# Kernel optimization log

Measured on AMD Instinct MI355X. Metric: run time of the kernel, lower is better.

## Reference

```python
import jax, jax.numpy as jnp
import numpy as np

N_NODES = 100000
N_EDGES = 1600000
D_NODE = 32
D_EDGE = 16
D_HID = 64
D_OUT = 32


def setup_inputs() -> dict:
    key = jax.random.key(0)
    ks = jax.random.split(key, 7)
    x = jax.random.normal(ks[0], (N_NODES, D_NODE), dtype=jnp.float32)
    edge_index = jax.random.randint(ks[1], (2, N_EDGES), 0, N_NODES, dtype=jnp.int64)
    edge_attr = jax.random.normal(ks[2], (N_EDGES, D_EDGE), dtype=jnp.float32)
    # 2-layer MLP params (Linear -> ReLU -> Linear), He-ish scaling
    W1 = jax.random.normal(ks[3], (D_NODE + D_EDGE, D_HID), dtype=jnp.float32) * (2.0 / (D_NODE + D_EDGE)) ** 0.5
    b1 = jnp.zeros((D_HID,), dtype=jnp.float32)
    W2 = jax.random.normal(ks[4], (D_HID, D_OUT), dtype=jnp.float32) * (2.0 / D_HID) ** 0.5
    b2 = jnp.zeros((D_OUT,), dtype=jnp.float32)
    return {"x": x, "edge_index": edge_index, "edge_attr": edge_attr,
            "W1": W1, "b1": b1, "W2": W2, "b2": b2}


def reference(x, edge_index, edge_attr, W1, b1, W2, b2):
    row, col = edge_index[0], edge_index[1]
    # gather source-node feats and concat with edge feats: [E, d_node + d_edge]
    inp = jnp.concatenate([x[col], edge_attr], axis=1)
    # 2-layer MLP over edges
    h = jax.nn.relu(inp @ W1 + b1)
    messages = h @ W2 + b2  # [E, d_out]
    # scatter-sum aggregate by destination node
    message = jax.ops.segment_sum(messages, row, num_segments=x.shape[0])
    return message
```

## Files before the change

kernel.cpp:

```cpp
#include <hip/hip_runtime.h>
#include <hip/hip_bf16.h>
#include <stdint.h>

#define N_NODES 100000
#define N_EDGES 1600000
#define D_NODE  32
#define D_EDGE  16
#define D_IN    48
#define D_HID   64
#define D_OUT   32

#define NBKT 98
#define BCAP 18432
#define SLICES (BCAP / 256)
#define S1_EDGES 1024
#define S1_NB 1563
#define SCAN_NB 391

#define CHUNKS_PER_BLOCK 4
#define BPB (SLICES / CHUNKS_PER_BLOCK)
#define MAXB_PER_XCD 13
#define AGG_GRID (8 * MAXB_PER_XCD * BPB)

#define NFLAGS_OFF  ((size_t)0)
#define NB1_OFF     ((size_t)64)
#define NB2_OFF     ((size_t)320)
#define W1BF_OFF    ((size_t)1024)
#define W2BF_OFF    ((size_t)9216)
#define GCUR_OFF    ((size_t)16384)
#define XBF_OFF     ((size_t)65536)
#define TMPH_OFF    ((size_t)8388608)
#define TMPE_OFF    ((size_t)16777216)
#define REC_OFF     ((size_t)75497472)
#define ACCUM_OFF   ((size_t)90177536)

typedef __attribute__((ext_vector_type(8))) short bf16x8;
typedef __attribute__((ext_vector_type(4))) float f32x4;

__device__ inline float bf2f(unsigned int u16) {
    return __uint_as_float(u16 << 16);
}
__device__ inline unsigned short f2bf_rne(float f) {
    unsigned int x = __float_as_uint(f);
    unsigned int r = (x + 0x7FFFu + ((x >> 16) & 1u)) >> 16;
    return (unsigned short)r;
}
__device__ inline unsigned int pk_bf2(float a, float b) {
    float2 f; f.x = a; f.y = b;
    __hip_bfloat162 h = __float22bfloat162_rn(f);
    return *reinterpret_cast<unsigned int*>(&h);
}
__device__ inline float ld_f(const void* p, int i, int isbf) {
    if (isbf) return bf2f(((const unsigned short*)p)[i]);
    return ((const float*)p)[i];
}

__global__ __launch_bounds__(256) void prep_kernel(
        const void* __restrict__ xq, const void* __restrict__ idxq,
        const void* __restrict__ W1q, const void* __restrict__ b1q,
        const void* __restrict__ W2q, const void* __restrict__ b2q,
        char* __restrict__ ws) {
    const int t = threadIdx.x;
    const int i0 = blockIdx.x * 256 + t;

    __shared__ int s_isbf;
    if (t < 64) {
        unsigned short u = ((const unsigned short*)xq)[t];
        unsigned long long mb = __ballot(((u >> 7) & 0xFF) >= 140);
        if (t == 0) s_isbf = (mb == 0ULL);
    }

    float4* acc4 = (float4*)(ws + ACCUM_OFF);
    float4 z; z.x = z.y = z.z = z.w = 0.0f;
    for (int i = i0; i < (N_NODES + 1) * 32 / 4; i += SCAN_NB * 256) acc4[i] = z;

    __syncthreads();
    const int isbf = s_isbf;

    unsigned short* xbf = (unsigned short*)(ws + XBF_OFF);
    for (int i = i0; i < N_NODES * 32 / 8; i += SCAN_NB * 256) {
        uint4 o;
        if (isbf) {
            o = ((const uint4*)xq)[i];
        } else {
            const float4* xp = (const float4*)xq + i * 2;
            float4 a = xp[0], b = xp[1];
            o.x = pk_bf2(a.x, a.y); o.y = pk_bf2(a.z, a.w);
            o.z = pk_bf2(b.x, b.y); o.w = pk_bf2(b.z, b.w);
        }
        ((uint4*)xbf)[i] = o;
    }

    if (blockIdx.x != 0) return;

    if (t < NBKT) ((int*)(ws + GCUR_OFF))[t] = t * BCAP;
    if (t < 64) {
        int wodd = ((const int*)idxq)[2 * t + 1];
        unsigned long long mi = __ballot(wodd != 0);
        if (t == 0) {
            int* flags = (int*)(ws + NFLAGS_OFF);
            flags[0] = isbf;
            flags[1] = (mi == 0ULL);
        }
    }

    float* b1 = (float*)(ws + NB1_OFF);
    float* b2 = (float*)(ws + NB2_OFF);
    unsigned short* w1b = (unsigned short*)(ws + W1BF_OFF);
    unsigned short* w2b = (unsigned short*)(ws + W2BF_OFF);

    if (t < D_HID) b1[t] = ld_f(b1q, t, isbf);
    if (t < D_OUT) b2[t] = ld_f(b2q, t, isbf);

    for (int i = t; i < D_HID * 64; i += 256) {
        int n = i >> 6, k = i & 63;
        float v = (k < D_IN) ? ld_f(W1q, k * D_HID + n, isbf) : 0.0f;
        w1b[i] = f2bf_rne(v);
    }
    for (int i = t; i < D_OUT * 64; i += 256) {
        int n = i >> 6, k = i & 63;
        w2b[i] = f2bf_rne(ld_f(W2q, k * D_OUT + n, isbf));
    }
}

#define PIDX(s) ((s) + ((s) >> 3))
__global__ __launch_bounds__(512) void partition_kernel(
        const void* __restrict__ idxq, const void* __restrict__ eaq,
        char* __restrict__ ws) {
    const int is64 = ((const int*)(ws + NFLAGS_OFF))[1];
    const int isbf = ((const int*)(ws + NFLAGS_OFF))[0];
    __shared__ int hist[128];
    __shared__ int sc[128];
    __shared__ int lofs[128];
    __shared__ int base[128];
    __shared__ int lcur[128];
    __shared__ unsigned int hdr[S1_EDGES];
    __shared__ unsigned char bkt[S1_EDGES];
    __shared__ __align__(16) uint4 pay[2][S1_EDGES + (S1_EDGES >> 3)];

    const int t = threadIdx.x;
    if (t < 128) hist[t] = 0;
    __syncthreads();

    const int e0 = blockIdx.x * S1_EDGES;
    const int total = min(N_EDGES - e0, S1_EDGES);

    int dstv[2];
#pragma unroll
    for (int i = 0; i < 2; ++i) {
        const int e = e0 + i * 512 + t;
        int dst = -1;
        if (e < N_EDGES) {
            if (is64) dst = (int)((const long long*)idxq)[e];
            else      dst = ((const int*)idxq)[e];
            atomicAdd(&hist[dst >> 10], 1);
        }
        dstv[i] = dst;
    }
    __syncthreads();

    if (t < 128) sc[t] = hist[t];
    __syncthreads();
    for (int d = 1; d < 128; d <<= 1) {
        int a = 0;
        if (t < 128 && t >= d) a = sc[t - d];
        __syncthreads();
        if (t < 128) sc[t] += a;
        __syncthreads();
    }
    if (t < 128) {
        lofs[t] = sc[t] - hist[t];
        lcur[t] = 0;
        if (t < NBKT) base[t] = atomicAdd((int*)(ws + GCUR_OFF) + t, hist[t]);
    }
    __syncthreads();

#pragma unroll
    for (int i = 0; i < 2; ++i) {
        const int e = e0 + i * 512 + t;
        if (e >= N_EDGES) continue;
        const int dst = dstv[i];
        int src;
        if (is64) src = (int)((const long long*)idxq)[N_EDGES + e];
        else      src = ((const int*)idxq)[N_EDGES + e];
        const int b = dst >> 10;
        const int r = atomicAdd(&lcur[b], 1);
        const int s = lofs[b] + r;
        hdr[s] = (unsigned)src | ((unsigned)(dst & 1023) << 17);
        bkt[s] = (unsigned char)b;

        uint4 u0, u1;
        if (isbf) {
            const uint4* p = (const uint4*)((const unsigned short*)eaq + (size_t)e * 16);
            u0 = p[0]; u1 = p[1];
        } else {
            const float4* p = (const float4*)((const float*)eaq + (size_t)e * 16);
            float4 a = p[0], b4 = p[1], c = p[2], d = p[3];
            u0.x = pk_bf2(a.x, a.y);  u0.y = pk_bf2(a.z, a.w);
            u0.z = pk_bf2(b4.x, b4.y); u0.w = pk_bf2(b4.z, b4.w);
            u1.x = pk_bf2(c.x, c.y);  u1.y = pk_bf2(c.z, c.w);
            u1.z = pk_bf2(d.x, d.y);  u1.w = pk_bf2(d.z, d.w);
        }
        pay[0][PIDX(s)] = u0;
        pay[1][PIDX(s)] = u1;
    }
    __syncthreads();

    unsigned int* tmph = (unsigned int*)(ws + TMPH_OFF);
    uint4*        tmp4 = (uint4*)(ws + TMPE_OFF);
    for (int s = t; s < total; s += 512) {
        const int b = bkt[s];
        const size_t g = (size_t)base[b] + (s - lofs[b]);
        tmph[g] = hdr[s];
        tmp4[g * 2]     = pay[0][PIDX(s)];
        tmp4[g * 2 + 1] = pay[1][PIDX(s)];
    }
}

__global__ __launch_bounds__(1024) void sort_kernel(char* __restrict__ ws) {
    __shared__ int hist[1024];
    __shared__ int cur[1024];
    const int b = blockIdx.x;
    const int t = threadIdx.x;
    hist[t] = 0;
    __syncthreads();

    const int cnt = ((const int*)(ws + GCUR_OFF))[b] - b * BCAP;
    const unsigned int* tmph = (const unsigned int*)(ws + TMPH_OFF) + (size_t)b * BCAP;
    unsigned long long* rec = (unsigned long long*)(ws + REC_OFF) + (size_t)b * BCAP;

    for (int i = t; i < cnt; i += 1024)
        atomicAdd(&hist[(tmph[i] >> 17) & 1023], 1);
    __syncthreads();

    int v = hist[t];
    for (int d = 1; d < 1024; d <<= 1) {
        int a = (t >= d) ? hist[t - d] : 0;
        __syncthreads();
        hist[t] += a;
        __syncthreads();
    }
    cur[t] = hist[t] - v;
    __syncthreads();

    for (int i = t; i < cnt; i += 1024) {
        unsigned int h = tmph[i];
        const int rd = (h >> 17) & 1023;
        const int rk = atomicAdd(&cur[rd], 1);
        unsigned long long out = ((unsigned long long)rd << 32)
                               | ((unsigned long long)(unsigned)i << 17)
                               | (h & 0x1FFFFu);
        rec[rk] = out;
    }
}

__global__ __launch_bounds__(256) void edge_mlp_agg_kernel(
        const char* __restrict__ wsro,
        float* __restrict__ accum) {
    const int xcd = blockIdx.x & 7;
    const int j   = blockIdx.x >> 3;
    const int m   = j / BPB;
    const int nb  = 12 + (xcd < 2);
    if (m >= nb) return;
    const int b      = xcd + (m << 3);
    const int slice0 = (j % BPB) * CHUNKS_PER_BLOCK;

    const int cnt = ((const int*)(wsro + GCUR_OFF))[b] - b * BCAP;
    if (slice0 * 256 >= cnt) return;

    __shared__ __align__(16) unsigned short hbuf[4][2][16][72];

    const int w   = threadIdx.x >> 6;
    const int l   = threadIdx.x & 63;
    const int m16 = l & 15;
    const int q   = l >> 4;

    const unsigned short* w1b = (const unsigned short*)(wsro + W1BF_OFF);
    const unsigned short* w2b = (const unsigned short*)(wsro + W2BF_OFF);
    const float* b1 = (const float*)(wsro + NB1_OFF);
    const float* b2 = (const float*)(wsro + NB2_OFF);
    const unsigned short* xbf  = (const unsigned short*)(wsro + XBF_OFF);
    const unsigned short* tmpe = (const unsigned short*)(wsro + TMPE_OFF) + (size_t)b * BCAP * 16;
    const unsigned long long* rec = (const unsigned long long*)(wsro + REC_OFF) + (size_t)b * BCAP;

    bf16x8 w1f[4][2], w2f[2][2];
#pragma unroll
    for (int t = 0; t < 4; ++t)
#pragma unroll
        for (int c = 0; c < 2; ++c)
            w1f[t][c] = *(const bf16x8*)(w1b + ((t * 16 + m16) * 64 + c * 32 + q * 8));
#pragma unroll
    for (int t = 0; t < 2; ++t)
#pragma unroll
        for (int c = 0; c < 2; ++c)
            w2f[t][c] = *(const bf16x8*)(w2b + ((t * 16 + m16) * 64 + c * 32 + q * 8));

    const float b1v[4] = { b1[m16], b1[16 + m16], b1[32 + m16], b1[48 + m16] };
    const float b2v[2] = { b2[m16], b2[16 + m16] };
    const int n0 = b << 10;

    for (int cc = 0; cc < CHUNKS_PER_BLOCK; ++cc) {
        const int kb = (slice0 + cc) * 256 + w * 64;
        if ((slice0 + cc) * 256 >= cnt) break;

        int srcv[4], tixv[4], dstv[4];
#pragma unroll
        for (int g = 0; g < 4; ++g) {
            const int p = kb + g * 16 + m16;
            unsigned long long r = rec[p];
            if (p < cnt) {
                unsigned int lo = (unsigned int)r;
                srcv[g] = (int)(lo & 0x1FFFFu);
                tixv[g] = (int)(lo >> 17);
                dstv[g] = n0 + (int)(r >> 32);
            } else {
                srcv[g] = 0;
                tixv[g] = 0;
                dstv[g] = N_NODES;
            }
        }

        bf16x8 A0[4], A1[4];
#pragma unroll
        for (int g = 0; g < 4; ++g) {
            A0[g] = *(const bf16x8*)(xbf  + (size_t)srcv[g] * D_NODE + q * 8);
            A1[g] = *(const bf16x8*)(tmpe + (size_t)tixv[g] * 16 + (q & 1) * 8);
        }

        auto L1 = [&](int g, int bb) {
#pragma unroll
            for (int t = 0; t < 4; ++t) {
                f32x4 c;
                c[0] = c[1] = c[2] = c[3] = b1v[t];
                c = __builtin_amdgcn_mfma_f32_16x16x32_bf16(A0[g], w1f[t][0], c, 0, 0, 0);
                c = __builtin_amdgcn_mfma_f32_16x16x32_bf16(A1[g], w1f[t][1], c, 0, 0, 0);
                unsigned int u0 = pk_bf2(fmaxf(c[0], 0.0f), fmaxf(c[1], 0.0f));
                unsigned int u1 = pk_bf2(fmaxf(c[2], 0.0f), fmaxf(c[3], 0.0f));
                hbuf[w][bb][q * 4 + 0][t * 16 + m16] = (unsigned short)u0;
                hbuf[w][bb][q * 4 + 1][t * 16 + m16] = (unsigned short)(u0 >> 16);
                hbuf[w][bb][q * 4 + 2][t * 16 + m16] = (unsigned short)u1;
                hbuf[w][bb][q * 4 + 3][t * 16 + m16] = (unsigned short)(u1 >> 16);
            }
        };

        auto L2R = [&](int g, int bb) {
            bf16x8 a20 = *(const bf16x8*)(&hbuf[w][bb][m16][q * 8]);
            bf16x8 a21 = *(const bf16x8*)(&hbuf[w][bb][m16][32 + q * 8]);
            f32x4 c0, c1;
            c0[0] = c0[1] = c0[2] = c0[3] = b2v[0];
            c1[0] = c1[1] = c1[2] = c1[3] = b2v[1];
            c0 = __builtin_amdgcn_mfma_f32_16x16x32_bf16(a20, w2f[0][0], c0, 0, 0, 0);
            c0 = __builtin_amdgcn_mfma_f32_16x16x32_bf16(a21, w2f[0][1], c0, 0, 0, 0);
            c1 = __builtin_amdgcn_mfma_f32_16x16x32_bf16(a20, w2f[1][0], c1, 0, 0, 0);
            c1 = __builtin_amdgcn_mfma_f32_16x16x32_bf16(a21, w2f[1][1], c1, 0, 0, 0);

            const int dstw = dstv[g];
            int dprev = __shfl(dstw, (m16 + 15) & 15, 16);
            bool isStart = (m16 == 0) || (dprev != dstw);
            unsigned long long bal = __ballot(isStart);
            unsigned mask16 = (unsigned)(bal >> (l & 48)) & 0xFFFFu;
            int start = 0;
            while (start < 16) {
                unsigned rest = mask16 >> 1 >> start;
                int next = rest ? (start + 1 + (int)__builtin_ctz(rest)) : 16;
                int d = __shfl(dstw, start, 16);
                float s0 = 0.0f, s1 = 0.0f;
#pragma unroll
                for (int r = 0; r < 4; ++r) {
                    int mm = q * 4 + r;
                    bool in = (mm >= start) && (mm < next);
                    s0 += in ? c0[r] : 0.0f;
                    s1 += in ? c1[r] : 0.0f;
                }
                s0 += __shfl_xor(s0, 16); s0 += __shfl_xor(s0, 32);
                s1 += __shfl_xor(s1, 16); s1 += __shfl_xor(s1, 32);
                if (q == 0) {
                    unsafeAtomicAdd(accum + (size_t)d * 32 + m16,      s0);
                    unsafeAtomicAdd(accum + (size_t)d * 32 + 16 + m16, s1);
                }
                start = next;
            }
        };

        L1(0, 0);
        L1(1, 1);
        L2R(0, 0);
        L1(2, 0);
        L2R(1, 1);
        L1(3, 1);
        L2R(2, 0);
        L2R(3, 1);
    }
}

__global__ __launch_bounds__(256) void convert_kernel(
        const char* __restrict__ wsro, const float* __restrict__ accum,
        void* __restrict__ out) {
    const int isbf = ((const int*)(wsro + NFLAGS_OFF))[0];
    const int i = blockIdx.x * 256 + threadIdx.x;
    float4 v = ((const float4*)accum)[i];
    if (isbf) {
        uint2 u;
        u.x = pk_bf2(v.x, v.y);
        u.y = pk_bf2(v.z, v.w);
        ((uint2*)out)[i] = u;
    } else {
        ((float4*)out)[i] = v;
    }
}

extern "C" void kernel_launch(void* const* d_in, const int* in_sizes, int n_in,
                              void* d_out, int out_size, void* d_ws, size_t ws_size,
                              hipStream_t stream) {
    const void* x   = d_in[0];
    const void* idx = d_in[1];
    const void* ea  = d_in[2];
    const void* W1  = d_in[3];
    const void* b1  = d_in[4];
    const void* W2  = d_in[5];
    const void* b2  = d_in[6];
    char* ws = (char*)d_ws;

    hipLaunchKernelGGL(prep_kernel, dim3(SCAN_NB), dim3(256), 0, stream,
                       x, idx, W1, b1, W2, b2, ws);

    hipLaunchKernelGGL(partition_kernel, dim3(S1_NB), dim3(512), 0, stream, idx, ea, ws);

    hipLaunchKernelGGL(sort_kernel, dim3(NBKT), dim3(1024), 0, stream, ws);

    hipLaunchKernelGGL(edge_mlp_agg_kernel, dim3(AGG_GRID), dim3(256), 0, stream,
                       (const char*)ws, (float*)(ws + ACCUM_OFF));

    hipLaunchKernelGGL(convert_kernel, dim3(N_NODES * 32 / 4 / 256), dim3(256), 0, stream,
                       (const char*)ws, (const float*)(ws + ACCUM_OFF), d_out);
}
```

Baseline: 324.5 us.

## Software-pipeline next chunk's record and feature gathers behind current MLP compute

Restructures the per-block chunk loop so the edge records and the gathered node/edge feature loads for chunk cc+1 are issued while chunk cc's MFMA layers and atomic scatter run. The intent is to hide global gather latency behind compute instead of stalling at the start of each chunk. In exchange it holds a second set of A0/A1 fragments and records in registers, which raises VGPR pressure and may lower occupancy.

```diff
diff --git a/kernel.cpp b/kernel.cpp
--- a/kernel.cpp
+++ b/kernel.cpp
@@ -267,6 +267,7 @@
 
     const int cnt = ((const int*)(wsro + GCUR_OFF))[b] - b * BCAP;
     if (slice0 * 256 >= cnt) return;
+    const int nchunk = min(CHUNKS_PER_BLOCK, (cnt - slice0 * 256 + 255) >> 8);
 
     __shared__ __align__(16) unsigned short hbuf[4][2][16][72];
 
@@ -299,97 +300,126 @@
     const float b2v[2] = { b2[m16], b2[16 + m16] };
     const int n0 = b << 10;
 
-    for (int cc = 0; cc < CHUNKS_PER_BLOCK; ++cc) {
-        const int kb = (slice0 + cc) * 256 + w * 64;
-        if ((slice0 + cc) * 256 >= cnt) break;
-
-        int srcv[4], tixv[4], dstv[4];
+    int dstv[4];
+    bf16x8 A0[4], A1[4];
+    unsigned long long rn[4];
+    bf16x8 A0n[4], A1n[4];
+
+    auto L1 = [&](int g, int bb) {
+#pragma unroll
+        for (int t = 0; t < 4; ++t) {
+            f32x4 c;
+            c[0] = c[1] = c[2] = c[3] = b1v[t];
+            c = __builtin_amdgcn_mfma_f32_16x16x32_bf16(A0[g], w1f[t][0], c, 0, 0, 0);
+            c = __builtin_amdgcn_mfma_f32_16x16x32_bf16(A1[g], w1f[t][1], c, 0, 0, 0);
+            unsigned int u0 = pk_bf2(fmaxf(c[0], 0.0f), fmaxf(c[1], 0.0f));
+            unsigned int u1 = pk_bf2(fmaxf(c[2], 0.0f), fmaxf(c[3], 0.0f));
+            hbuf[w][bb][q * 4 + 0][t * 16 + m16] = (unsigned short)u0;
+            hbuf[w][bb][q * 4 + 1][t * 16 + m16] = (unsigned short)(u0 >> 16);
+            hbuf[w][bb][q * 4 + 2][t * 16 + m16] = (unsigned short)u1;
+            hbuf[w][bb][q * 4 + 3][t * 16 + m16] = (unsigned short)(u1 >> 16);
+        }
+    };
+
+    auto L2R = [&](int g, int bb) {
+        bf16x8 a20 = *(const bf16x8*)(&hbuf[w][bb][m16][q * 8]);
+        bf16x8 a21 = *(const bf16x8*)(&hbuf[w][bb][m16][32 + q * 8]);
+        f32x4 c0, c1;
+        c0[0] = c0[1] = c0[2] = c0[3] = b2v[0];
+        c1[0] = c1[1] = c1[2] = c1[3] = b2v[1];
+        c0 = __builtin_amdgcn_mfma_f32_16x16x32_bf16(a20, w2f[0][0], c0, 0, 0, 0);
+        c0 = __builtin_amdgcn_mfma_f32_16x16x32_bf16(a21, w2f[0][1], c0, 0, 0, 0);
+        c1 = __builtin_amdgcn_mfma_f32_16x16x32_bf16(a20, w2f[1][0], c1, 0, 0, 0);
+        c1 = __builtin_amdgcn_mfma_f32_16x16x32_bf16(a21, w2f[1][1], c1, 0, 0, 0);
+
+        const int dstw = dstv[g];
+        int dprev = __shfl(dstw, (m16 + 15) & 15, 16);
+        bool isStart = (m16 == 0) || (dprev != dstw);
+        unsigned long long bal = __ballot(isStart);
+        unsigned mask16 = (unsigned)(bal >> (l & 48)) & 0xFFFFu;
+        int start = 0;
+        while (start < 16) {
+            unsigned rest = mask16 >> 1 >> start;
+            int next = rest ? (start + 1 + (int)__builtin_ctz(rest)) : 16;
+            int d = __shfl(dstw, start, 16);
+            float s0 = 0.0f, s1 = 0.0f;
+#pragma unroll
+            for (int r = 0; r < 4; ++r) {
+                int mm = q * 4 + r;
+                bool in = (mm >= start) && (mm < next);
+                s0 += in ? c0[r] : 0.0f;
+                s1 += in ? c1[r] : 0.0f;
+            }
+            s0 += __shfl_xor(s0, 16); s0 += __shfl_xor(s0, 32);
+            s1 += __shfl_xor(s1, 16); s1 += __shfl_xor(s1, 32);
+            if (q == 0) {
+                unsafeAtomicAdd(accum + (size_t)d * 32 + m16,      s0);
+                unsafeAtomicAdd(accum + (size_t)d * 32 + 16 + m16, s1);
+            }
+            start = next;
+        }
+    };
+
+    {
+        const int kb = slice0 * 256 + w * 64;
 #pragma unroll
         for (int g = 0; g < 4; ++g) {
             const int p = kb + g * 16 + m16;
             unsigned long long r = rec[p];
+            int sv = 0, tv = 0, dv = N_NODES;
             if (p < cnt) {
                 unsigned int lo = (unsigned int)r;
-                srcv[g] = (int)(lo & 0x1FFFFu);
-                tixv[g] = (int)(lo >> 17);
-                dstv[g] = n0 + (int)(r >> 32);
-            } else {
-                srcv[g] = 0;
-                tixv[g] = 0;
-                dstv[g] = N_NODES;
+                sv = (int)(lo & 0x1FFFFu);
+                tv = (int)(lo >> 17);
+                dv = n0 + (int)(r >> 32);
             }
-        }
-
-        bf16x8 A0[4], A1[4];
-#pragma unroll
-        for (int g = 0; g < 4; ++g) {
-            A0[g] = *(const bf16x8*)(xbf  + (size_t)srcv[g] * D_NODE + q * 8);
-            A1[g] = *(const bf16x8*)(tmpe + (size_t)tixv[g] * 16 + (q & 1) * 8);
-        }
-
-        auto L1 = [&](int g, int bb) {
-#pragma unroll
-            for (int t = 0; t < 4; ++t) {
-                f32x4 c;
-                c[0] = c[1] = c[2] = c[3] = b1v[t];
-                c = __builtin_amdgcn_mfma_f32_16x16x32_bf16(A0[g], w1f[t][0], c, 0, 0, 0);
-                c = __builtin_amdgcn_mfma_f32_16x16x32_bf16(A1[g], w1f[t][1], c, 0, 0, 0);
-                unsigned int u0 = pk_bf2(fmaxf(c[0], 0.0f), fmaxf(c[1], 0.0f));
-                unsigned int u1 = pk_bf2(fmaxf(c[2], 0.0f), fmaxf(c[3], 0.0f));
-                hbuf[w][bb][q * 4 + 0][t * 16 + m16] = (unsigned short)u0;
-                hbuf[w][bb][q * 4 + 1][t * 16 + m16] = (unsigned short)(u0 >> 16);
-                hbuf[w][bb][q * 4 + 2][t * 16 + m16] = (unsigned short)u1;
-                hbuf[w][bb][q * 4 + 3][t * 16 + m16] = (unsigned short)(u1 >> 16);
-            }
-        };
-
-        auto L2R = [&](int g, int bb) {
-            bf16x8 a20 = *(const bf16x8*)(&hbuf[w][bb][m16][q * 8]);
-            bf16x8 a21 = *(const bf16x8*)(&hbuf[w][bb][m16][32 + q * 8]);
-            f32x4 c0, c1;
-            c0[0] = c0[1] = c0[2] = c0[3] = b2v[0];
-            c1[0] = c1[1] = c1[2] = c1[3] = b2v[1];
-            c0 = __builtin_amdgcn_mfma_f32_16x16x32_bf16(a20, w2f[0][0], c0, 0, 0, 0);
-            c0 = __builtin_amdgcn_mfma_f32_16x16x32_bf16(a21, w2f[0][1], c0, 0, 0, 0);
-            c1 = __builtin_amdgcn_mfma_f32_16x16x32_bf16(a20, w2f[1][0], c1, 0, 0, 0);
-            c1 = __builtin_amdgcn_mfma_f32_16x16x32_bf16(a21, w2f[1][1], c1, 0, 0, 0);
-
-            const int dstw = dstv[g];
-            int dprev = __shfl(dstw, (m16 + 15) & 15, 16);
-            bool isStart = (m16 == 0) || (dprev != dstw);
-            unsigned long long bal = __ballot(isStart);
-            unsigned mask16 = (unsigned)(bal >> (l & 48)) & 0xFFFFu;
-            int start = 0;
-            while (start < 16) {
-                unsigned rest = mask16 >> 1 >> start;
-                int next = rest ? (start + 1 + (int)__builtin_ctz(rest)) : 16;
-                int d = __shfl(dstw, start, 16);
-                float s0 = 0.0f, s1 = 0.0f;
-#pragma unroll
-                for (int r = 0; r < 4; ++r) {
-                    int mm = q * 4 + r;
-                    bool in = (mm >= start) && (mm < next);
-                    s0 += in ? c0[r] : 0.0f;
-                    s1 += in ? c1[r] : 0.0f;
-                }
-                s0 += __shfl_xor(s0, 16); s0 += __shfl_xor(s0, 32);
-                s1 += __shfl_xor(s1, 16); s1 += __shfl_xor(s1, 32);
-                if (q == 0) {
-                    unsafeAtomicAdd(accum + (size_t)d * 32 + m16,      s0);
-                    unsafeAtomicAdd(accum + (size_t)d * 32 + 16 + m16, s1);
-                }
-                start = next;
-            }
-        };
+            dstv[g] = dv;
+            A0[g] = *(const bf16x8*)(xbf  + (size_t)sv * D_NODE + q * 8);
+            A1[g] = *(const bf16x8*)(tmpe + (size_t)tv * 16 + (q & 1) * 8);
+        }
+    }
+
+    for (int cc = 0; cc < nchunk; ++cc) {
+        const bool hasNext = (cc + 1 < nchunk);
+        const int kbn = (slice0 + cc + 1) * 256 + w * 64;
+
+        if (hasNext) {
+#pragma unroll
+            for (int g = 0; g < 4; ++g)
+                rn[g] = rec[kbn + g * 16 + m16];
+        }
 
         L1(0, 0);
         L1(1, 1);
         L2R(0, 0);
+
+        if (hasNext) {
+#pragma unroll
+            for (int g = 0; g < 4; ++g) {
+                const int p = kbn + g * 16 + m16;
+                unsigned int lo = (unsigned int)rn[g];
+                int sv = (p < cnt) ? (int)(lo & 0x1FFFFu) : 0;
+                int tv = (p < cnt) ? (int)(lo >> 17) : 0;
+                A0n[g] = *(const bf16x8*)(xbf  + (size_t)sv * D_NODE + q * 8);
+                A1n[g] = *(const bf16x8*)(tmpe + (size_t)tv * 16 + (q & 1) * 8);
+            }
+        }
+
         L1(2, 0);
         L2R(1, 1);
         L1(3, 1);
         L2R(2, 0);
         L2R(3, 1);
+
+        if (hasNext) {
+#pragma unroll
+            for (int g = 0; g < 4; ++g) {
+                const int p = kbn + g * 16 + m16;
+                A0[g] = A0n[g];
+                A1[g] = A1n[g];
+                dstv[g] = (p < cnt) ? (n0 + (int)(rn[g] >> 32)) : N_NODES;
+            }
+        }
     }
 }
 
```

Measured after the change: 332.8 us. 2.5% more time.

## Fold prep kernel into partition and sort kernels, memset bucket counters

Applied to the files above, without the earlier changes.

Removes the standalone prep kernel. Accumulator zeroing, x-to-bf16 conversion and format detection now run inside the partition kernel, and weight/bias conversion runs in an extra block of the sort kernel. Bucket cursors are zeroed with a memset and the bucket base offset is added in the kernel, which drops one full kernel launch and its serialization barrier. The cost is that every partition block redundantly detects input formats and does strided zero/convert work before its own edge work, and one extra memset node is added.

```diff
diff --git a/kernel.cpp b/kernel.cpp
--- a/kernel.cpp
+++ b/kernel.cpp
@@ -15,7 +15,6 @@
 #define SLICES (BCAP / 256)
 #define S1_EDGES 1024
 #define S1_NB 1563
-#define SCAN_NB 391
 
 #define CHUNKS_PER_BLOCK 4
 #define BPB (SLICES / CHUNKS_PER_BLOCK)
@@ -55,80 +54,11 @@
     return ((const float*)p)[i];
 }
 
-__global__ __launch_bounds__(256) void prep_kernel(
-        const void* __restrict__ xq, const void* __restrict__ idxq,
-        const void* __restrict__ W1q, const void* __restrict__ b1q,
-        const void* __restrict__ W2q, const void* __restrict__ b2q,
-        char* __restrict__ ws) {
-    const int t = threadIdx.x;
-    const int i0 = blockIdx.x * 256 + t;
-
-    __shared__ int s_isbf;
-    if (t < 64) {
-        unsigned short u = ((const unsigned short*)xq)[t];
-        unsigned long long mb = __ballot(((u >> 7) & 0xFF) >= 140);
-        if (t == 0) s_isbf = (mb == 0ULL);
-    }
-
-    float4* acc4 = (float4*)(ws + ACCUM_OFF);
-    float4 z; z.x = z.y = z.z = z.w = 0.0f;
-    for (int i = i0; i < (N_NODES + 1) * 32 / 4; i += SCAN_NB * 256) acc4[i] = z;
-
-    __syncthreads();
-    const int isbf = s_isbf;
-
-    unsigned short* xbf = (unsigned short*)(ws + XBF_OFF);
-    for (int i = i0; i < N_NODES * 32 / 8; i += SCAN_NB * 256) {
-        uint4 o;
-        if (isbf) {
-            o = ((const uint4*)xq)[i];
-        } else {
-            const float4* xp = (const float4*)xq + i * 2;
-            float4 a = xp[0], b = xp[1];
-            o.x = pk_bf2(a.x, a.y); o.y = pk_bf2(a.z, a.w);
-            o.z = pk_bf2(b.x, b.y); o.w = pk_bf2(b.z, b.w);
-        }
-        ((uint4*)xbf)[i] = o;
-    }
-
-    if (blockIdx.x != 0) return;
-
-    if (t < NBKT) ((int*)(ws + GCUR_OFF))[t] = t * BCAP;
-    if (t < 64) {
-        int wodd = ((const int*)idxq)[2 * t + 1];
-        unsigned long long mi = __ballot(wodd != 0);
-        if (t == 0) {
-            int* flags = (int*)(ws + NFLAGS_OFF);
-            flags[0] = isbf;
-            flags[1] = (mi == 0ULL);
-        }
-    }
-
-    float* b1 = (float*)(ws + NB1_OFF);
-    float* b2 = (float*)(ws + NB2_OFF);
-    unsigned short* w1b = (unsigned short*)(ws + W1BF_OFF);
-    unsigned short* w2b = (unsigned short*)(ws + W2BF_OFF);
-
-    if (t < D_HID) b1[t] = ld_f(b1q, t, isbf);
-    if (t < D_OUT) b2[t] = ld_f(b2q, t, isbf);
-
-    for (int i = t; i < D_HID * 64; i += 256) {
-        int n = i >> 6, k = i & 63;
-        float v = (k < D_IN) ? ld_f(W1q, k * D_HID + n, isbf) : 0.0f;
-        w1b[i] = f2bf_rne(v);
-    }
-    for (int i = t; i < D_OUT * 64; i += 256) {
-        int n = i >> 6, k = i & 63;
-        w2b[i] = f2bf_rne(ld_f(W2q, k * D_OUT + n, isbf));
-    }
-}
-
 #define PIDX(s) ((s) + ((s) >> 3))
 __global__ __launch_bounds__(512) void partition_kernel(
         const void* __restrict__ idxq, const void* __restrict__ eaq,
-        char* __restrict__ ws) {
-    const int is64 = ((const int*)(ws + NFLAGS_OFF))[1];
-    const int isbf = ((const int*)(ws + NFLAGS_OFF))[0];
+        const void* __restrict__ xq, char* __restrict__ ws) {
+    __shared__ int s_flags;
     __shared__ int hist[128];
     __shared__ int sc[128];
     __shared__ int lofs[128];
@@ -139,8 +69,41 @@
     __shared__ __align__(16) uint4 pay[2][S1_EDGES + (S1_EDGES >> 3)];
 
     const int t = threadIdx.x;
+    const int i0 = blockIdx.x * 512 + t;
+
+    if (t < 64) {
+        unsigned short u = ((const unsigned short*)xq)[t];
+        unsigned long long mb = __ballot(((u >> 7) & 0xFF) >= 140);
+        int wodd = ((const int*)idxq)[2 * t + 1];
+        unsigned long long mi = __ballot(wodd != 0);
+        if (t == 0) s_flags = (mb == 0ULL ? 1 : 0) | (mi == 0ULL ? 2 : 0);
+    }
     if (t < 128) hist[t] = 0;
-    __syncthreads();
+
+    {
+        float4* acc4 = (float4*)(ws + ACCUM_OFF);
+        float4 z; z.x = z.y = z.z = z.w = 0.0f;
+        for (int i = i0; i < (N_NODES + 1) * 32 / 4; i += S1_NB * 512) acc4[i] = z;
+    }
+    __syncthreads();
+    const int isbf = s_flags & 1;
+    const int is64 = (s_flags >> 1) & 1;
+
+    {
+        unsigned short* xbf = (unsigned short*)(ws + XBF_OFF);
+        for (int i = i0; i < N_NODES * 32 / 8; i += S1_NB * 512) {
+            uint4 o;
+            if (isbf) {
+                o = ((const uint4*)xq)[i];
+            } else {
+                const float4* xp = (const float4*)xq + i * 2;
+                float4 a = xp[0], b = xp[1];
+                o.x = pk_bf2(a.x, a.y); o.y = pk_bf2(a.z, a.w);
+                o.z = pk_bf2(b.x, b.y); o.w = pk_bf2(b.z, b.w);
+            }
+            ((uint4*)xbf)[i] = o;
+        }
+    }
 
     const int e0 = blockIdx.x * S1_EDGES;
     const int total = min(N_EDGES - e0, S1_EDGES);
@@ -171,7 +134,8 @@
     if (t < 128) {
         lofs[t] = sc[t] - hist[t];
         lcur[t] = 0;
-        if (t < NBKT) base[t] = atomicAdd((int*)(ws + GCUR_OFF) + t, hist[t]);
+        if (t < NBKT)
+            base[t] = t * BCAP + atomicAdd((int*)(ws + GCUR_OFF) + t, hist[t]);
     }
     __syncthreads();
 
@@ -210,22 +174,57 @@
     uint4*        tmp4 = (uint4*)(ws + TMPE_OFF);
     for (int s = t; s < total; s += 512) {
         const int b = bkt[s];
-        const size_t g = (size_t)base[b] + (s - lofs[b]);
-        tmph[g] = hdr[s];
-        tmp4[g * 2]     = pay[0][PIDX(s)];
-        tmp4[g * 2 + 1] = pay[1][PIDX(s)];
-    }
-}
-
-__global__ __launch_bounds__(1024) void sort_kernel(char* __restrict__ ws) {
+        const size_t g = (size_t)(b * BCAP) + base[b] - b * BCAP + (s - lofs[b]);
+        tmph[(size_t)base[b] + (s - lofs[b])] = hdr[s];
+        tmp4[((size_t)base[b] + (s - lofs[b])) * 2]     = pay[0][PIDX(s)];
+        tmp4[((size_t)base[b] + (s - lofs[b])) * 2 + 1] = pay[1][PIDX(s)];
+        (void)g;
+    }
+}
+
+__global__ __launch_bounds__(1024) void sort_kernel(
+        const void* __restrict__ xq,
+        const void* __restrict__ W1q, const void* __restrict__ b1q,
+        const void* __restrict__ W2q, const void* __restrict__ b2q,
+        char* __restrict__ ws) {
+    const int b = blockIdx.x;
+    const int t = threadIdx.x;
+
+    if (b == NBKT) {
+        __shared__ int s_isbf;
+        if (t < 64) {
+            unsigned short u = ((const unsigned short*)xq)[t];
+            unsigned long long mb = __ballot(((u >> 7) & 0xFF) >= 140);
+            if (t == 0) s_isbf = (mb == 0ULL);
+        }
+        __syncthreads();
+        const int isbf = s_isbf;
+        if (t == 0) ((int*)(ws + NFLAGS_OFF))[0] = isbf;
+
+        float* b1 = (float*)(ws + NB1_OFF);
+        float* b2 = (float*)(ws + NB2_OFF);
+        unsigned short* w1b = (unsigned short*)(ws + W1BF_OFF);
+        unsigned short* w2b = (unsigned short*)(ws + W2BF_OFF);
+        if (t < D_HID) b1[t] = ld_f(b1q, t, isbf);
+        if (t < D_OUT) b2[t] = ld_f(b2q, t, isbf);
+        for (int i = t; i < D_HID * 64; i += 1024) {
+            int n = i >> 6, k = i & 63;
+            float v = (k < D_IN) ? ld_f(W1q, k * D_HID + n, isbf) : 0.0f;
+            w1b[i] = f2bf_rne(v);
+        }
+        for (int i = t; i < D_OUT * 64; i += 1024) {
+            int n = i >> 6, k = i & 63;
+            w2b[i] = f2bf_rne(ld_f(W2q, k * D_OUT + n, isbf));
+        }
+        return;
+    }
+
     __shared__ int hist[1024];
     __shared__ int cur[1024];
-    const int b = blockIdx.x;
-    const int t = threadIdx.x;
     hist[t] = 0;
     __syncthreads();
 
-    const int cnt = ((const int*)(ws + GCUR_OFF))[b] - b * BCAP;
+    const int cnt = ((const int*)(ws + GCUR_OFF))[b];
     const unsigned int* tmph = (const unsigned int*)(ws + TMPH_OFF) + (size_t)b * BCAP;
     unsigned long long* rec = (unsigned long long*)(ws + REC_OFF) + (size_t)b * BCAP;
 
@@ -265,7 +264,7 @@
     const int b      = xcd + (m << 3);
     const int slice0 = (j % BPB) * CHUNKS_PER_BLOCK;
 
-    const int cnt = ((const int*)(wsro + GCUR_OFF))[b] - b * BCAP;
+    const int cnt = ((const int*)(wsro + GCUR_OFF))[b];
     if (slice0 * 256 >= cnt) return;
 
     __shared__ __align__(16) unsigned short hbuf[4][2][16][72];
@@ -421,12 +420,13 @@
     const void* b2  = d_in[6];
     char* ws = (char*)d_ws;
 
-    hipLaunchKernelGGL(prep_kernel, dim3(SCAN_NB), dim3(256), 0, stream,
-                       x, idx, W1, b1, W2, b2, ws);
-
-    hipLaunchKernelGGL(partition_kernel, dim3(S1_NB), dim3(512), 0, stream, idx, ea, ws);
-
-    hipLaunchKernelGGL(sort_kernel, dim3(NBKT), dim3(1024), 0, stream, ws);
+    hipMemsetAsync(ws + GCUR_OFF, 0, NBKT * sizeof(int), stream);
+
+    hipLaunchKernelGGL(partition_kernel, dim3(S1_NB), dim3(512), 0, stream,
+                       idx, ea, x, ws);
+
+    hipLaunchKernelGGL(sort_kernel, dim3(NBKT + 1), dim3(1024), 0, stream,
+                       x, W1, b1, W2, b2, ws);
 
     hipLaunchKernelGGL(edge_mlp_agg_kernel, dim3(AGG_GRID), dim3(256), 0, stream,
                        (const char*)ws, (float*)(ws + ACCUM_OFF));
```

After: 323.1 us. About the same (-0.5%).
